# Kernel tuning notes

Hardware: AMD Instinct MI355X
Metric: run time of the kernel (lower is better)

Reference implementation:

```python
import jax, jax.numpy as jnp
import numpy as np

B, C, H, W = 8, 256, 64, 64
HEADS, PTS = 8, 4
HD = C // HEADS
CIN_G, CIN_S, COUT = 1024, 320, 320


def _sine_pe(c, h, w):
    # LoFTR-style 2D sinusoidal position encoding, returns [C,H,W]
    pe = np.zeros((c, h, w), dtype=np.float32)
    y = np.broadcast_to(np.arange(h, dtype=np.float32)[None, :, None], (1, h, w))
    x = np.broadcast_to(np.arange(w, dtype=np.float32)[None, None, :], (1, h, w))
    div = np.exp(np.arange(0, c // 2, 2, dtype=np.float32) * (-np.log(10000.0) / (c // 2)))[:, None, None]
    pe[0::4] = np.sin(x * div)
    pe[1::4] = np.cos(x * div)
    pe[2::4] = np.sin(y * div)
    pe[3::4] = np.cos(y * div)
    return jnp.asarray(pe)


def _ref_points(h, w):
    # faithful to source: meshgrid over (W,H) 'ij', stack (col,row), flatten w-major
    rows = np.linspace(0, 1, w, dtype=np.float32)
    cols = np.linspace(0, 1, h, dtype=np.float32)
    R, Cg = np.meshgrid(rows, cols, indexing='ij')  # [W,H]
    return jnp.asarray(np.stack([Cg, R], -1).reshape(-1, 2))  # [W*H,2]


PE = _sine_pe(C, H, W)
RP = _ref_points(H, W)


def conv1x1(x, w, b):
    return jnp.einsum('bchw,oc->bohw', x, w) + b[None, :, None, None]


def deform_attn(qf, vf, vp_w, vp_b, so_w, so_b, aw_w, aw_b, op_w, op_b):
    # qf: [B,Nq,C]  vf: [B,Nv,C]  (single level, H x W value map)
    Bn, Nq, Cc = qf.shape
    v = (vf @ vp_w + vp_b).reshape(Bn, -1, HEADS, HD).transpose(0, 2, 1, 3)  # [B,h,Nv,hd]
    off = (qf @ so_w + so_b).reshape(Bn, Nq, HEADS, PTS, 2)
    aw = jax.nn.softmax((qf @ aw_w + aw_b).reshape(Bn, Nq, HEADS, PTS), axis=-1)
    loc = RP[None, :, None, None, :] + off / jnp.array([W, H], qf.dtype)  # [B,Nq,h,P,2]
    # grid_sample align_corners=False, zero padding
    px = loc[..., 0] * W - 0.5
    py = loc[..., 1] * H - 0.5
    x0 = jnp.floor(px).astype(jnp.int32)
    y0 = jnp.floor(py).astype(jnp.int32)
    wx = px - x0
    wy = py - y0
    out = jnp.zeros((Bn, HEADS, Nq, PTS, HD), qf.dtype)
    for dx, dy, wgt in ((0, 0, (1 - wx) * (1 - wy)), (1, 0, wx * (1 - wy)),
                        (0, 1, (1 - wx) * wy), (1, 1, wx * wy)):
        xi = x0 + dx
        yi = y0 + dy
        valid = ((xi >= 0) & (xi < W) & (yi >= 0) & (yi < H)).astype(qf.dtype)
        idx = jnp.clip(yi, 0, H - 1) * W + jnp.clip(xi, 0, W - 1)  # [B,Nq,h,P]
        idx_h = idx.transpose(0, 2, 1, 3).reshape(Bn, HEADS, Nq * PTS)
        g = jnp.take_along_axis(v, idx_h[..., None], axis=2).reshape(Bn, HEADS, Nq, PTS, HD)
        out = out + g * (wgt * valid).transpose(0, 2, 1, 3)[..., None]
    o = (out * aw.transpose(0, 2, 1, 3)[..., None]).sum(3)  # [B,h,Nq,hd]
    o = o.transpose(0, 2, 1, 3).reshape(Bn, Nq, Cc)
    return o @ op_w + op_b + qf  # mmcv: output_proj + identity (dropout=eval)


def cross_attn(q, value, vp_w, vp_b, so_w, so_b, aw_w, aw_b, op_w, op_b):
    qp = q + PE[None]  # query += pe
    qf = qp.reshape(qp.shape[0], C, H * W).transpose(0, 2, 1)
    vf = value.reshape(value.shape[0], C, H * W).transpose(0, 2, 1)
    o = deform_attn(qf, vf, vp_w, vp_b, so_w, so_b, aw_w, aw_b, op_w, op_b)
    o = o.transpose(0, 2, 1).reshape(qp.shape)
    return o + qp


def setup_inputs() -> dict:
    key = jax.random.key(0)
    ks = jax.random.split(key, 40)
    inp = {}
    inp['ground'] = jax.random.normal(ks[0], (B, CIN_G, H, W), jnp.float32)
    inp['sat'] = jax.random.normal(ks[1], (B, CIN_S, H, W), jnp.float32)
    inp['osm'] = jax.random.normal(ks[2], (B, CIN_S, H, W), jnp.float32)
    i = [3]
    def p(name, shape, scale=0.02):
        inp[name] = jax.random.normal(ks[i[0]], shape, jnp.float32) * scale
        i[0] += 1
    p('gc_w', (C, CIN_G)); p('gc_b', (C,))
    p('sc_w', (C, CIN_S)); p('sc_b', (C,))
    p('up_w', (COUT, C)); p('up_b', (COUT,))
    p('a_w1', (C, 64)); p('a_b1', (64,))
    p('a_w2', (64, 1)); p('a_b2', (1,))
    for pre in ('sat_', 'osm_'):
        p(pre + 'vp_w', (C, C)); p(pre + 'vp_b', (C,))
        p(pre + 'so_w', (C, HEADS * PTS * 2)); p(pre + 'so_b', (HEADS * PTS * 2,))
        p(pre + 'aw_w', (C, HEADS * PTS)); p(pre + 'aw_b', (HEADS * PTS,))
        p(pre + 'op_w', (C, C)); p(pre + 'op_b', (C,))
    inp['index'] = 0
    return inp


def reference(ground, sat, osm, gc_w, gc_b, sc_w, sc_b, up_w, up_b,
              a_w1, a_b1, a_w2, a_b2,
              sat_vp_w, sat_vp_b, sat_so_w, sat_so_b, sat_aw_w, sat_aw_b, sat_op_w, sat_op_b,
              osm_vp_w, osm_vp_b, osm_so_w, osm_so_b, osm_aw_w, osm_aw_b, osm_op_w, osm_op_b,
              index):
    del index  # params for index=0 already selected
    g = conv1x1(ground, gc_w, gc_b)
    s = conv1x1(sat, sc_w, sc_b)
    o = conv1x1(osm, sc_w, sc_b)  # source bug: osm projected with sat_convs
    gf = g.reshape(B, C, H * W).transpose(0, 2, 1)
    alpha = jax.nn.sigmoid(jax.nn.relu(gf @ a_w1 + a_b1) @ a_w2 + a_b2)  # [B,Nq,1]
    a = alpha.mean(axis=1)[:, :, None, None]  # [B,1,1,1]
    sat_out = cross_attn(g, s, sat_vp_w, sat_vp_b, sat_so_w, sat_so_b, sat_aw_w, sat_aw_b, sat_op_w, sat_op_b)
    # torch in-place `query += pe` inside ca_sat mutates `ground`, so ca_osm sees g + PE
    osm_out = cross_attn(g + PE[None], o, osm_vp_w, osm_vp_b, osm_so_w, osm_so_b, osm_aw_w, osm_aw_b, osm_op_w, osm_op_b)
    fused = a * sat_out + (1.0 - a) * osm_out
    return conv1x1(fused, up_w, up_b), a
```

## Files before the change

kernel.cpp:

```cpp
#include <hip/hip_runtime.h>
#include <cstddef>
#include <cstdint>

#define NB 8
#define NQ 4096

typedef __attribute__((ext_vector_type(8))) short bfrag8;
typedef __attribute__((ext_vector_type(4))) float facc4;
typedef __attribute__((ext_vector_type(4))) unsigned short us4;
typedef __attribute__((ext_vector_type(8))) unsigned short us8;

__device__ __forceinline__ float bf2f(unsigned short u) {
  union { unsigned int i; float f; } v; v.i = ((unsigned int)u) << 16; return v.f;
}
__device__ __forceinline__ unsigned short f2bf(float f) {
  union { float f; unsigned int i; } v; v.f = f;
  unsigned int r = v.i + 0x7FFFu + ((v.i >> 16) & 1u);
  return (unsigned short)(r >> 16);
}
__device__ __forceinline__ void gload16(const void* g, void* l) {
  __builtin_amdgcn_global_load_lds(
      (const __attribute__((address_space(1))) void*)g,
      (__attribute__((address_space(3))) void*)l, 16, 0, 0);
}

struct PrepArgs {
  const float *gc_w, *up_w, *up_b;
  const float *so_w0, *so_b0, *so_w1, *so_b1;
  const float *aw_w0, *aw_b0, *aw_w1, *aw_b1;
  const float *op_w0, *op_w1;
  unsigned short *PET, *WG, *WUP, *OPT0, *OPT1, *SOW0, *SOW1;
  float *BUPP, *SOB0, *SOB1;
};

__global__ __launch_bounds__(256) void mega_prep(PrepArgs p) {
  const int blk = blockIdx.x, t = threadIdx.x;
  if (blk < 4096) {
    int idx = blk * 256 + t;
    int q = idx >> 8, c = idx & 255;
    int h = q >> 6, w = q & 63;
    int k = c >> 2, m = c & 3;
    float dv = expf((float)(2 * k) * (-9.210340371976184f / 128.0f));
    float arg = ((m < 2) ? (float)w : (float)h) * dv;
    p.PET[idx] = f2bf(((m & 1) == 0) ? sinf(arg) : cosf(arg));
  } else if (blk < 5120) {
    int i = (blk - 4096) * 256 + t;
    p.WG[i] = f2bf(p.gc_w[i]);
  } else if (blk < 5504) {
    int i = (blk - 5120) * 256 + t;
    int m = i >> 8, k = i & 255;
    p.WUP[i] = (m < 320) ? f2bf(p.up_w[m * 256 + k]) : 0;
  } else if (blk < 5505) {
    p.BUPP[t] = (t < 320) ? p.up_b[t] : 0.f;
    if (t < 128) {
      int i2 = 256 + t;
      p.BUPP[i2] = (i2 < 320) ? p.up_b[i2] : 0.f;
    }
  } else if (blk < 6017) {
    int i = (blk - 5505) * 256 + t;
    int which = i >> 16, j = i & 65535;
    int o = j >> 8, k = j & 255;
    (which ? p.OPT1 : p.OPT0)[j] = f2bf((which ? p.op_w1 : p.op_w0)[k * 256 + o]);
  } else {
    int i = (blk - 6017) * 256 + t;
    int which = i >> 15, j = i & 32767;
    int row = j >> 8, k = j & 255;
    const float* sw = which ? p.so_w1 : p.so_w0;
    const float* aw = which ? p.aw_w1 : p.aw_w0;
    float v = 0.f;
    if (row < 64) v = sw[k * 64 + row];
    else if (row < 96) v = aw[k * 32 + (row - 64)];
    (which ? p.SOW1 : p.SOW0)[j] = f2bf(v);
    if (j < 128) {
      const float* sb = which ? p.so_b1 : p.so_b0;
      const float* ab = which ? p.aw_b1 : p.aw_b0;
      (which ? p.SOB1 : p.SOB0)[j] = (j < 64) ? sb[j] : ((j < 96) ? ab[j - 64] : 0.f);
    }
  }
}

__global__ __launch_bounds__(256) void k_wv(const float* __restrict__ vp_w0,
                                            const float* __restrict__ vp_b0,
                                            const float* __restrict__ vp_w1,
                                            const float* __restrict__ vp_b1,
                                            const float* __restrict__ sc_w,
                                            const float* __restrict__ sc_b,
                                            unsigned short* __restrict__ WV0,
                                            unsigned short* __restrict__ WV1,
                                            float* __restrict__ BV0,
                                            float* __restrict__ BV1) {
  const int br = blockIdx.y, kt = blockIdx.x, k0 = kt * 20, t = threadIdx.x;
  const float* vp = br ? vp_w1 : vp_w0;
  unsigned short* WV = br ? WV1 : WV0;
  __shared__ float vt[32][256];
  __shared__ float st[32][20];
  __shared__ float sb[32];
  float acc[20] = {};
  float accB = 0.f;
  for (int c0 = 0; c0 < 256; c0 += 32) {
    __syncthreads();
#pragma unroll
    for (int cc = 0; cc < 32; ++cc)
      vt[cc][t] = vp[(size_t)(c0 + cc) * 256 + t];
    for (int i = t; i < 640; i += 256)
      st[i / 20][i % 20] = sc_w[(size_t)(c0 + i / 20) * 320 + k0 + (i % 20)];
    if (t < 32) sb[t] = sc_b[c0 + t];
    __syncthreads();
#pragma unroll
    for (int cc = 0; cc < 32; ++cc) {
      float v = vt[cc][t];
      accB = fmaf(v, sb[cc], accB);
#pragma unroll
      for (int j = 0; j < 20; ++j)
        acc[j] = fmaf(v, st[cc][j], acc[j]);
    }
  }
#pragma unroll
  for (int j = 0; j < 20; ++j) WV[(size_t)t * 320 + k0 + j] = f2bf(acc[j]);
  if (kt == 0) (br ? BV1 : BV0)[t] = (br ? vp_b1 : vp_b0)[t] + accB;
}

struct GArgs {
  const unsigned short* W[2];
  const unsigned short* X[2];
  const float* bias[2];
  void* out[2];
  const unsigned short* res[2];
  float rscale[2];
  int K, ldm, bmask, brshift;
};
template <int MODE>
__global__ __launch_bounds__(256) void gemm_bf16(GArgs g) {
  __shared__ unsigned short As[8192];
  __shared__ unsigned short Bs[8192];
  const int t = threadIdx.x;
  const int lane = t & 63, w = t >> 6;
  const int z = blockIdx.z;
  const int b = z & g.bmask, br = z >> g.brshift;
  const int K = g.K;
  const int n0 = blockIdx.x * 128, m0 = 0;
  const unsigned short* W = g.W[br];
  const unsigned short* Xb = g.X[br] + (size_t)b * NQ * K;

  const unsigned short* asrc[4];
  const unsigned short* bsrc[4];
  unsigned short* adst[4];
  unsigned short* bdst[4];
#pragma unroll
  for (int i = 0; i < 4; ++i) {
    int cid = i * 256 + t;
    int row = cid >> 3;
    int cc = (cid & 7) ^ (row & 7);
    asrc[i] = W + (size_t)(m0 + row) * K + cc * 8;
    bsrc[i] = Xb + (size_t)(n0 + row) * K + cc * 8;
    adst[i] = &As[i * 2048 + w * 512];
    bdst[i] = &Bs[i * 2048 + w * 512];
  }
  const int wm = (w >> 1) * 64, wn = (w & 1) * 64;
  const int l15 = lane & 15, l4 = lane >> 4;
  facc4 acc[4][4];
#pragma unroll
  for (int i = 0; i < 4; ++i)
#pragma unroll
    for (int j = 0; j < 4; ++j) acc[i][j] = facc4{0.f, 0.f, 0.f, 0.f};

  for (int k0 = 0; k0 < K; k0 += 64) {
    if (k0) __syncthreads();
#pragma unroll
    for (int i = 0; i < 4; ++i) {
      gload16(asrc[i], adst[i]);
      gload16(bsrc[i], bdst[i]);
      asrc[i] += 64; bsrc[i] += 64;
    }
    __syncthreads();
#pragma unroll
    for (int kk = 0; kk < 2; ++kk) {
      bfrag8 af[4], bf[4];
#pragma unroll
      for (int mi = 0; mi < 4; ++mi) {
        int row = wm + mi * 16 + l15;
        af[mi] = *reinterpret_cast<const bfrag8*>(&As[row * 64 + (((kk * 4 + l4) ^ (row & 7)) * 8)]);
      }
#pragma unroll
      for (int ni = 0; ni < 4; ++ni) {
        int row = wn + ni * 16 + l15;
        bf[ni] = *reinterpret_cast<const bfrag8*>(&Bs[row * 64 + (((kk * 4 + l4) ^ (row & 7)) * 8)]);
      }
#pragma unroll
      for (int mi = 0; mi < 4; ++mi)
#pragma unroll
        for (int ni = 0; ni < 4; ++ni)
          acc[mi][ni] = __builtin_amdgcn_mfma_f32_16x16x32_bf16(af[mi], bf[ni], acc[mi][ni], 0, 0, 0);
    }
  }
  const size_t bq = (size_t)b * NQ;
#pragma unroll
  for (int mi = 0; mi < 4; ++mi) {
#pragma unroll
    for (int ni = 0; ni < 4; ++ni) {
      int m = m0 + wm + mi * 16 + l4 * 4;
      int n = n0 + wn + ni * 16 + l15;
      facc4 v = acc[mi][ni];
      unsigned short* o16 = (unsigned short*)g.out[br];
      float rv[4] = {v[0], v[1], v[2], v[3]};
      if constexpr (MODE == 1) {
        float sc = g.rscale[br];
        float4 bv = *reinterpret_cast<const float4*>(&g.bias[br][m]);
        rv[0] = rv[0] * sc + bv.x; rv[1] = rv[1] * sc + bv.y;
        rv[2] = rv[2] * sc + bv.z; rv[3] = rv[3] * sc + bv.w;
      }
      if constexpr (MODE == 2) {
        float sc = g.rscale[br];
        us4 rr = *reinterpret_cast<const us4*>(&g.res[br][(size_t)n * 128 + m]);
#pragma unroll
        for (int r = 0; r < 4; ++r) rv[r] += sc * bf2f(rr[r]);
      }
      us4 pk;
#pragma unroll
      for (int r = 0; r < 4; ++r) pk[r] = f2bf(rv[r]);
      *reinterpret_cast<us4*>(&o16[(bq + n) * g.ldm + m]) = pk;
    }
  }
}

struct NArgs {
  const unsigned short* W[2];
  const void* X[2];
  const float* bias[2];
  void* out[2];
  const unsigned short* G;
  const unsigned short* PET;
  const float* afin;
  float rs[2];
  int K, zmask, zshift;
};
template <int BSRC, int MODE>
__global__ __launch_bounds__(256) void gemm_n64(NArgs g) {
  __shared__ unsigned short As[16384];
  __shared__ unsigned short Bs[4096];
  const int t = threadIdx.x;
  const int lane = t & 63, w = t >> 6;
  const int z = blockIdx.z;
  const int b = z & g.zmask, br = z >> g.zshift;
  const int K = g.K;
  const int n0 = blockIdx.x * 64;

  const unsigned short* W = g.W[br];
  const unsigned short* asrc[8];
  unsigned short* adst[8];
#pragma unroll
  for (int i = 0; i < 8; ++i) {
    int c = t + 256 * i;
    int row = c >> 3;
    int k8 = (c & 7) ^ (row & 7);
    asrc[i] = W + (size_t)row * K + k8 * 8;
    adst[i] = &As[w * 512 + i * 2048];
  }

  const unsigned short* bsrc16[2];
  unsigned short* bdst16[2];
  const float* bsrcf = nullptr;
  const int kb = t >> 4, nb = t & 15;
  if constexpr (BSRC == 0) {
    const unsigned short* Xh = (const unsigned short*)g.X[br];
#pragma unroll
    for (int i = 0; i < 2; ++i) {
      int c = t + 256 * i;
      int n = c >> 3;
      int k8 = (c & 7) ^ (n & 7);
      bsrc16[i] = Xh + ((size_t)b * NQ + n0 + n) * K + k8 * 8;
      bdst16[i] = &Bs[w * 512 + i * 2048];
    }
  } else {
    const float* Xf = (const float*)g.X[br];
    bsrcf = Xf + (size_t)b * K * NQ + (size_t)(kb * 4) * NQ + n0 + nb * 4;
  }

  const int l15 = lane & 15, l4 = lane >> 4;
  facc4 acc[4][4];
#pragma unroll
  for (int i = 0; i < 4; ++i)
#pragma unroll
    for (int j = 0; j < 4; ++j) acc[i][j] = facc4{0.f, 0.f, 0.f, 0.f};

  for (int k0 = 0; k0 < K; k0 += 64) {
    if (k0) __syncthreads();
#pragma unroll
    for (int i = 0; i < 8; ++i) {
      gload16(asrc[i], adst[i]);
      asrc[i] += 64;
    }
    if constexpr (BSRC == 0) {
      gload16(bsrc16[0], bdst16[0]); bsrc16[0] += 64;
      gload16(bsrc16[1], bdst16[1]); bsrc16[1] += 64;
    } else {
      float vv[4][4];
#pragma unroll
      for (int r = 0; r < 4; ++r) {
        float4 v = *reinterpret_cast<const float4*>(bsrcf + (size_t)k0 * NQ + (size_t)r * NQ);
        vv[r][0] = v.x; vv[r][1] = v.y; vv[r][2] = v.z; vv[r][3] = v.w;
      }
#pragma unroll
      for (int c = 0; c < 4; ++c) {
        int n = nb * 4 + c;
        us4 pk;
        pk[0] = f2bf(vv[0][c]); pk[1] = f2bf(vv[1][c]);
        pk[2] = f2bf(vv[2][c]); pk[3] = f2bf(vv[3][c]);
        int off = n * 64 + (((kb >> 1) ^ (n & 7)) * 8) + (kb & 1) * 4;
        *reinterpret_cast<us4*>(&Bs[off]) = pk;
      }
    }
    __syncthreads();
#pragma unroll
    for (int kk = 0; kk < 2; ++kk) {
      bfrag8 af[4], bf[4];
#pragma unroll
      for (int mi = 0; mi < 4; ++mi) {
        int row = w * 64 + mi * 16 + l15;
        af[mi] = *reinterpret_cast<const bfrag8*>(&As[row * 64 + (((kk * 4 + l4) ^ (row & 7)) * 8)]);
      }
#pragma unroll
      for (int ni = 0; ni < 4; ++ni) {
        int row = ni * 16 + l15;
        bf[ni] = *reinterpret_cast<const bfrag8*>(&Bs[row * 64 + (((kk * 4 + l4) ^ (row & 7)) * 8)]);
      }
#pragma unroll
      for (int mi = 0; mi < 4; ++mi)
#pragma unroll
        for (int ni = 0; ni < 4; ++ni)
          acc[mi][ni] = __builtin_amdgcn_mfma_f32_16x16x32_bf16(af[mi], bf[ni], acc[mi][ni], 0, 0, 0);
    }
  }

  const size_t bq = (size_t)b * NQ;
  unsigned short* o16 = (unsigned short*)g.out[br];
#pragma unroll
  for (int mi = 0; mi < 4; ++mi) {
#pragma unroll
    for (int ni = 0; ni < 4; ++ni) {
      int m = w * 64 + mi * 16 + l4 * 4;
      int n = n0 + ni * 16 + l15;
      facc4 v = acc[mi][ni];
      float4 bv = *reinterpret_cast<const float4*>(&g.bias[br][m]);
      float rv[4] = {v[0] + bv.x, v[1] + bv.y, v[2] + bv.z, v[3] + bv.w};
      if constexpr (MODE == 6) {
        float a = g.afin[b];
        float s = br ? (1.f - a) : a;
        float rsc = g.rs[br];
        us4 gv = *reinterpret_cast<const us4*>(&g.G[(bq + n) * 256 + m]);
        us4 pv = *reinterpret_cast<const us4*>(&g.PET[(size_t)n * 256 + m]);
#pragma unroll
        for (int r = 0; r < 4; ++r)
          rv[r] = s * (rv[r] + 2.f * bf2f(gv[r]) + rsc * bf2f(pv[r]));
      }
      us4 pk;
#pragma unroll
      for (int r = 0; r < 4; ++r) pk[r] = f2bf(rv[r]);
      *reinterpret_cast<us4*>(&o16[(bq + n) * 256 + m]) = pk;
    }
  }
}

__global__ __launch_bounds__(384) void gemm_up(const unsigned short* __restrict__ W,
                                               const unsigned short* __restrict__ S0,
                                               const unsigned short* __restrict__ S1,
                                               const float* __restrict__ bias,
                                               float* __restrict__ out) {
  __shared__ unsigned short As[24576];
  __shared__ unsigned short Bs[4096];
  const int t = threadIdx.x;
  const int lane = t & 63, w = t >> 6;
  const int b = blockIdx.z;
  const int n0 = blockIdx.x * 64;

  const unsigned short* asrc[8];
  unsigned short* adst[8];
#pragma unroll
  for (int i = 0; i < 8; ++i) {
    int c = t + 384 * i;
    int row = c >> 3;
    int k8 = (c & 7) ^ (row & 7);
    asrc[i] = W + (size_t)row * 256 + k8 * 8;
    adst[i] = &As[w * 512 + i * 3072];
  }
  const bool bst = t < 256;
  size_t bidx[2];
  int bn[2];
  if (bst) {
#pragma unroll
    for (int i = 0; i < 2; ++i) {
      int c = t + 256 * i;
      bn[i] = c >> 3;
      int bk8 = (c & 7) ^ (bn[i] & 7);
      bidx[i] = ((size_t)b * NQ + n0 + bn[i]) * 256 + bk8 * 8;
    }
  }

  const int l15 = lane & 15, l4 = lane >> 4;
  facc4 acc[4][4];
#pragma unroll
  for (int i = 0; i < 4; ++i)
#pragma unroll
    for (int j = 0; j < 4; ++j) acc[i][j] = facc4{0.f, 0.f, 0.f, 0.f};

  for (int k0 = 0; k0 < 256; k0 += 64) {
    if (k0) __syncthreads();
#pragma unroll
    for (int i = 0; i < 8; ++i) {
      gload16(asrc[i], adst[i]);
      asrc[i] += 64;
    }
    if (bst) {
#pragma unroll
      for (int i = 0; i < 2; ++i) {
        us8 x = *reinterpret_cast<const us8*>(&S0[bidx[i] + k0]);
        us8 y = *reinterpret_cast<const us8*>(&S1[bidx[i] + k0]);
        us8 o;
#pragma unroll
        for (int j = 0; j < 8; ++j) o[j] = f2bf(bf2f(x[j]) + bf2f(y[j]));
        *reinterpret_cast<us8*>(&Bs[(t + 256 * i) * 8]) = o;
      }
    }
    __syncthreads();
#pragma unroll
    for (int kk = 0; kk < 2; ++kk) {
      bfrag8 af[4], bf[4];
#pragma unroll
      for (int mi = 0; mi < 4; ++mi) {
        int row = w * 64 + mi * 16 + l15;
        af[mi] = *reinterpret_cast<const bfrag8*>(&As[row * 64 + (((kk * 4 + l4) ^ (row & 7)) * 8)]);
      }
#pragma unroll
      for (int ni = 0; ni < 4; ++ni) {
        int row = ni * 16 + l15;
        bf[ni] = *reinterpret_cast<const bfrag8*>(&Bs[row * 64 + (((kk * 4 + l4) ^ (row & 7)) * 8)]);
      }
#pragma unroll
      for (int mi = 0; mi < 4; ++mi)
#pragma unroll
        for (int ni = 0; ni < 4; ++ni)
          acc[mi][ni] = __builtin_amdgcn_mfma_f32_16x16x32_bf16(af[mi], bf[ni], acc[mi][ni], 0, 0, 0);
    }
  }
#pragma unroll
  for (int mi = 0; mi < 4; ++mi) {
    int m = w * 64 + mi * 16 + l4 * 4;
    if (m >= 320) continue;
#pragma unroll
    for (int ni = 0; ni < 4; ++ni) {
      int n = n0 + ni * 16 + l15;
      facc4 v = acc[mi][ni];
#pragma unroll
      for (int r = 0; r < 4; ++r)
        out[((size_t)b * 320 + m + r) * NQ + n] = v[r] + bias[m + r];
    }
  }
}

__global__ __launch_bounds__(256) void k_alpha(const unsigned short* __restrict__ G,
                                               const float* __restrict__ w1,
                                               const float* __restrict__ b1,
                                               const float* __restrict__ w2,
                                               const float* __restrict__ b2,
                                               float* __restrict__ partial) {
  int b = blockIdx.y;
  int qbase = blockIdx.x * 16;
  __shared__ float gs[16][256];
  __shared__ float wsum[4];
  int t = threadIdx.x;
  const unsigned short* gp = G + ((size_t)b * NQ + qbase) * 256;
#pragma unroll
  for (int i = t; i < 512; i += 256) {
    bfrag8 v = *reinterpret_cast<const bfrag8*>(&gp[i * 8]);
    int row = i >> 5, col = (i & 31) * 8;
#pragma unroll
    for (int j = 0; j < 8; ++j) gs[row][col + j] = bf2f((unsigned short)v[j]);
  }
  __syncthreads();
  int wv = t >> 6, lane = t & 63;
  float a0 = 0.f, a1 = 0.f, a2 = 0.f, a3 = 0.f;
  const float* g0 = gs[wv * 4 + 0];
  const float* g1 = gs[wv * 4 + 1];
  const float* g2 = gs[wv * 4 + 2];
  const float* g3 = gs[wv * 4 + 3];
#pragma unroll 4
  for (int k = 0; k < 256; ++k) {
    float wk = w1[k * 64 + lane];
    a0 = fmaf(g0[k], wk, a0); a1 = fmaf(g1[k], wk, a1);
    a2 = fmaf(g2[k], wk, a2); a3 = fmaf(g3[k], wk, a3);
  }
  float b1l = b1[lane], w2l = w2[lane];
  a0 = fmaxf(a0 + b1l, 0.f) * w2l; a1 = fmaxf(a1 + b1l, 0.f) * w2l;
  a2 = fmaxf(a2 + b1l, 0.f) * w2l; a3 = fmaxf(a3 + b1l, 0.f) * w2l;
#pragma unroll
  for (int off = 32; off; off >>= 1) {
    a0 += __shfl_xor(a0, off); a1 += __shfl_xor(a1, off);
    a2 += __shfl_xor(a2, off); a3 += __shfl_xor(a3, off);
  }
  if (lane == 0) {
    float bb = b2[0];
    float s = 1.f / (1.f + expf(-(a0 + bb))) + 1.f / (1.f + expf(-(a1 + bb))) +
              1.f / (1.f + expf(-(a2 + bb))) + 1.f / (1.f + expf(-(a3 + bb)));
    wsum[wv] = s;
  }
  __syncthreads();
  if (t == 0) partial[(size_t)b * 256 + blockIdx.x] = wsum[0] + wsum[1] + wsum[2] + wsum[3];
}

__global__ __launch_bounds__(256) void k_alpha_fin(const float* __restrict__ partial,
                                                   float* __restrict__ afin,
                                                   float* __restrict__ out_a) {
  int b = blockIdx.x;
  __shared__ float sm[256];
  sm[threadIdx.x] = partial[(size_t)b * 256 + threadIdx.x];
  __syncthreads();
  for (int st = 128; st; st >>= 1) {
    if (threadIdx.x < st) sm[threadIdx.x] += sm[threadIdx.x + st];
    __syncthreads();
  }
  if (threadIdx.x == 0) {
    float a = sm[0] * (1.f / 4096.f);
    afin[b] = a;
    out_a[b] = a;
  }
}

__global__ __launch_bounds__(256) void k_sample(const unsigned short* __restrict__ VP0,
                                                const unsigned short* __restrict__ VP1,
                                                const unsigned short* __restrict__ SWb,
                                                unsigned short* __restrict__ OATT0,
                                                unsigned short* __restrict__ OATT1) {
  int y = blockIdx.y;
  int b = y & 7, br = y >> 3;
  int q0 = blockIdx.x * 8;
  const unsigned short* VP = (br ? VP1 : VP0) + (size_t)b * NQ * 256;
  const unsigned short* SWp = SWb + (((size_t)br * NB + b) * NQ + q0) * 128;
  unsigned short* OATT = (br ? OATT1 : OATT0) + ((size_t)b * NQ + q0) * 256;
  __shared__ unsigned short sws[1024];
  int t = threadIdx.x;
  *reinterpret_cast<us4*>(&sws[t * 4]) = *reinterpret_cast<const us4*>(&SWp[t * 4]);
  __syncthreads();
  int qi = t >> 5, ss = t & 31, head = ss >> 2, hdg = ss & 3;
  int q = q0 + qi;
  const unsigned short* sw = &sws[qi * 128];
  float l0 = bf2f(sw[64 + head * 4 + 0]);
  float l1 = bf2f(sw[64 + head * 4 + 1]);
  float l2 = bf2f(sw[64 + head * 4 + 2]);
  float l3 = bf2f(sw[64 + head * 4 + 3]);
  float mx = fmaxf(fmaxf(l0, l1), fmaxf(l2, l3));
  float e0 = expf(l0 - mx), e1 = expf(l1 - mx), e2 = expf(l2 - mx), e3 = expf(l3 - mx);
  float inv = 1.f / (e0 + e1 + e2 + e3);
  float aw[4] = {e0 * inv, e1 * inv, e2 * inv, e3 * inv};
  float rpx = (float)(q & 63) * (64.f / 63.f) - 0.5f;
  float rpy = (float)(q >> 6) * (64.f / 63.f) - 0.5f;
  const unsigned short* vb = VP + head * 32 + hdg * 8;
  float acc[8] = {};
#pragma unroll
  for (int p = 0; p < 4; ++p) {
    float px = rpx + bf2f(sw[head * 8 + p * 2 + 0]);
    float py = rpy + bf2f(sw[head * 8 + p * 2 + 1]);
    float fx = floorf(px), fy = floorf(py);
    int x0 = (int)fx, y0 = (int)fy;
    float wx = px - fx, wy = py - fy;
#pragma unroll
    for (int dy = 0; dy < 2; ++dy) {
#pragma unroll
      for (int dx = 0; dx < 2; ++dx) {
        int xi = x0 + dx, yi = y0 + dy;
        if (xi >= 0 && xi < 64 && yi >= 0 && yi < 64) {
          float wa = aw[p] * (dx ? wx : 1.f - wx) * (dy ? wy : 1.f - wy);
          bfrag8 v = *reinterpret_cast<const bfrag8*>(&vb[(size_t)(yi * 64 + xi) * 256]);
#pragma unroll
          for (int j = 0; j < 8; ++j) acc[j] = fmaf(wa, bf2f((unsigned short)v[j]), acc[j]);
        }
      }
    }
  }
  us8 o;
#pragma unroll
  for (int j = 0; j < 8; ++j) o[j] = f2bf(acc[j]);
  *reinterpret_cast<us8*>(&OATT[qi * 256 + ss * 8]) = o;
}

extern "C" void kernel_launch(void* const* d_in, const int* in_sizes, int n_in,
                              void* d_out, int out_size, void* d_ws, size_t ws_size,
                              hipStream_t stream) {
  const float* ground = (const float*)d_in[0];
  const float* sat = (const float*)d_in[1];
  const float* osm = (const float*)d_in[2];
  const float* gc_w = (const float*)d_in[3];
  const float* gc_b = (const float*)d_in[4];
  const float* sc_w = (const float*)d_in[5];
  const float* sc_b = (const float*)d_in[6];
  const float* up_w = (const float*)d_in[7];
  const float* up_b = (const float*)d_in[8];
  const float* a_w1 = (const float*)d_in[9];
  const float* a_b1 = (const float*)d_in[10];
  const float* a_w2 = (const float*)d_in[11];
  const float* a_b2 = (const float*)d_in[12];
  const float* vp_w[2] = {(const float*)d_in[13], (const float*)d_in[21]};
  const float* vp_b[2] = {(const float*)d_in[14], (const float*)d_in[22]};
  const float* so_w[2] = {(const float*)d_in[15], (const float*)d_in[23]};
  const float* so_b[2] = {(const float*)d_in[16], (const float*)d_in[24]};
  const float* aw_w[2] = {(const float*)d_in[17], (const float*)d_in[25]};
  const float* aw_b[2] = {(const float*)d_in[18], (const float*)d_in[26]};
  const float* op_w[2] = {(const float*)d_in[19], (const float*)d_in[27]};
  const float* op_b[2] = {(const float*)d_in[20], (const float*)d_in[28]};

  char* wsb = (char*)d_ws;
  const size_t MBy = 1 << 20;
  unsigned short* PET  = (unsigned short*)(wsb);
  unsigned short* WG   = (unsigned short*)(wsb + 2 * MBy);
  unsigned short* WV0  = (unsigned short*)(wsb + 2 * MBy + 524288);
  unsigned short* WV1  = (unsigned short*)(wsb + 2 * MBy + 786432);
  unsigned short* WUP  = (unsigned short*)(wsb + 3 * MBy);
  unsigned short* OPT0 = (unsigned short*)(wsb + 3 * MBy + 262144);
  unsigned short* OPT1 = (unsigned short*)(wsb + 3 * MBy + 393216);
  unsigned short* SOW0 = (unsigned short*)(wsb + 3 * MBy + 524288);
  unsigned short* SOW1 = (unsigned short*)(wsb + 3 * MBy + 589824);
  unsigned short* PESO0 = (unsigned short*)(wsb + 4 * MBy);
  unsigned short* PESO1 = (unsigned short*)(wsb + 5 * MBy);
  float* SOB0 = (float*)(wsb + 6 * MBy);
  float* SOB1 = (float*)(wsb + 6 * MBy + 4096);
  float* BV0  = (float*)(wsb + 6 * MBy + 8192);
  float* BV1  = (float*)(wsb + 6 * MBy + 12288);
  float* BUPP = (float*)(wsb + 6 * MBy + 16384);
  float* PART = (float*)(wsb + 6 * MBy + 32768);
  float* AFIN = (float*)(wsb + 6 * MBy + 65536);
  unsigned short* G     = (unsigned short*)(wsb + 8 * MBy);
  unsigned short* VP0b  = (unsigned short*)(wsb + 24 * MBy);
  unsigned short* VP1b  = (unsigned short*)(wsb + 40 * MBy);
  unsigned short* SW    = (unsigned short*)(wsb + 56 * MBy);
  unsigned short* OATT0 = (unsigned short*)(wsb + 72 * MBy);
  unsigned short* OATT1 = (unsigned short*)(wsb + 88 * MBy);
  unsigned short* SATO  = (unsigned short*)(wsb + 104 * MBy);
  unsigned short* OSMO  = (unsigned short*)(wsb + 120 * MBy);

  float* out32 = (float*)d_out;
  float* out_a = out32 + (size_t)NB * 320 * NQ;

  dim3 blk(256);

  {
    PrepArgs p;
    p.gc_w = gc_w; p.up_w = up_w; p.up_b = up_b;
    p.so_w0 = so_w[0]; p.so_b0 = so_b[0]; p.so_w1 = so_w[1]; p.so_b1 = so_b[1];
    p.aw_w0 = aw_w[0]; p.aw_b0 = aw_b[0]; p.aw_w1 = aw_w[1]; p.aw_b1 = aw_b[1];
    p.op_w0 = op_w[0]; p.op_w1 = op_w[1];
    p.PET = PET; p.WG = WG; p.WUP = WUP;
    p.OPT0 = OPT0; p.OPT1 = OPT1; p.SOW0 = SOW0; p.SOW1 = SOW1;
    p.BUPP = BUPP; p.SOB0 = SOB0; p.SOB1 = SOB1;
    mega_prep<<<dim3(6273), blk, 0, stream>>>(p);
  }
  k_wv<<<dim3(16, 2), blk, 0, stream>>>(vp_w[0], vp_b[0], vp_w[1], vp_b[1],
                                        sc_w, sc_b, WV0, WV1, BV0, BV1);

  {
    GArgs a = {};
    a.W[0] = SOW0; a.W[1] = SOW1;
    a.X[0] = PET;  a.X[1] = PET;
    a.bias[0] = SOB0; a.bias[1] = SOB1;
    a.out[0] = PESO0; a.out[1] = PESO1;
    a.rscale[0] = 1.f; a.rscale[1] = 2.f;
    a.K = 256; a.ldm = 128; a.bmask = 0; a.brshift = 0;
    gemm_bf16<1><<<dim3(32, 1, 2), blk, 0, stream>>>(a);
  }

  {
    NArgs a = {};
    a.W[0] = WG; a.W[1] = WG;
    a.X[0] = ground; a.X[1] = ground;
    a.bias[0] = gc_b; a.bias[1] = gc_b;
    a.out[0] = G; a.out[1] = G;
    a.K = 1024; a.zmask = 7; a.zshift = 31;
    gemm_n64<1, 0><<<dim3(64, 1, NB), blk, 0, stream>>>(a);
  }

  k_alpha<<<dim3(256, NB), blk, 0, stream>>>(G, a_w1, a_b1, a_w2, a_b2, PART);
  k_alpha_fin<<<dim3(NB), blk, 0, stream>>>(PART, AFIN, out_a);

  {
    GArgs a = {};
    a.W[0] = SOW0; a.W[1] = SOW1;
    a.X[0] = G; a.X[1] = G;
    a.out[0] = SW; a.out[1] = SW + (size_t)NB * NQ * 128;
    a.res[0] = PESO0; a.res[1] = PESO1;
    a.rscale[0] = 1.f; a.rscale[1] = 1.f;
    a.K = 256; a.ldm = 128; a.bmask = 7; a.brshift = 3;
    gemm_bf16<2><<<dim3(32, 1, 16), blk, 0, stream>>>(a);
  }

  {
    NArgs a = {};
    a.W[0] = WV0; a.W[1] = WV1;
    a.X[0] = sat; a.X[1] = osm;
    a.bias[0] = BV0; a.bias[1] = BV1;
    a.out[0] = VP0b; a.out[1] = VP1b;
    a.K = 320; a.zmask = 7; a.zshift = 3;
    gemm_n64<1, 0><<<dim3(64, 1, 16), blk, 0, stream>>>(a);
  }

  k_sample<<<dim3(512, 16), blk, 0, stream>>>(VP0b, VP1b, SW, OATT0, OATT1);

  {
    NArgs a = {};
    a.W[0] = OPT0; a.W[1] = OPT1;
    a.X[0] = OATT0; a.X[1] = OATT1;
    a.bias[0] = op_b[0]; a.bias[1] = op_b[1];
    a.out[0] = SATO; a.out[1] = OSMO;
    a.G = G; a.PET = PET; a.afin = AFIN;
    a.rs[0] = 2.f; a.rs[1] = 4.f;
    a.K = 256; a.zmask = 7; a.zshift = 3;
    gemm_n64<0, 6><<<dim3(64, 1, 16), blk, 0, stream>>>(a);
  }

  gemm_up<<<dim3(64, 1, NB), dim3(384), 0, stream>>>(WUP, SATO, OSMO, BUPP, out32);
}
```

Measured before the change: 299.0 us.

## Fuse deformable sampling, output projection and branch blend into one tail kernel

Replaces the separate sampling kernel and the output-projection GEMM with a single kernel. It gathers bilinear samples into LDS, multiplies them by the projection weights for both branches, and writes the alpha-blended fused result. The final upsampling GEMM now loads one precomputed fused tensor directly into LDS instead of adding two branch outputs. This removes several large intermediate round-trips through global memory and two launches. In exchange the grid is much smaller and each block uses a lot of LDS, so latency hiding for the gather may suffer.

Result: slower. 385.5 us (+28.9%).

```diff
diff --git a/kernel.cpp b/kernel.cpp
--- a/kernel.cpp
+++ b/kernel.cpp
@@ -138,7 +138,7 @@
   const int z = blockIdx.z;
   const int b = z & g.bmask, br = z >> g.brshift;
   const int K = g.K;
-  const int n0 = blockIdx.x * 128, m0 = 0;
+  const int n0 = blockIdx.x * 128;
   const unsigned short* W = g.W[br];
   const unsigned short* Xb = g.X[br] + (size_t)b * NQ * K;
 
@@ -151,7 +151,7 @@
     int cid = i * 256 + t;
     int row = cid >> 3;
     int cc = (cid & 7) ^ (row & 7);
-    asrc[i] = W + (size_t)(m0 + row) * K + cc * 8;
+    asrc[i] = W + (size_t)row * K + cc * 8;
     bsrc[i] = Xb + (size_t)(n0 + row) * K + cc * 8;
     adst[i] = &As[i * 2048 + w * 512];
     bdst[i] = &Bs[i * 2048 + w * 512];
@@ -198,7 +198,7 @@
   for (int mi = 0; mi < 4; ++mi) {
 #pragma unroll
     for (int ni = 0; ni < 4; ++ni) {
-      int m = m0 + wm + mi * 16 + l4 * 4;
+      int m = wm + mi * 16 + l4 * 4;
       int n = n0 + wn + ni * 16 + l15;
       facc4 v = acc[mi][ni];
       unsigned short* o16 = (unsigned short*)g.out[br];
@@ -228,13 +228,8 @@
   const void* X[2];
   const float* bias[2];
   void* out[2];
-  const unsigned short* G;
-  const unsigned short* PET;
-  const float* afin;
-  float rs[2];
   int K, zmask, zshift;
 };
-template <int BSRC, int MODE>
 __global__ __launch_bounds__(256) void gemm_n64(NArgs g) {
   __shared__ unsigned short As[16384];
   __shared__ unsigned short Bs[4096];
@@ -257,24 +252,9 @@
     adst[i] = &As[w * 512 + i * 2048];
   }
 
-  const unsigned short* bsrc16[2];
-  unsigned short* bdst16[2];
-  const float* bsrcf = nullptr;
   const int kb = t >> 4, nb = t & 15;
-  if constexpr (BSRC == 0) {
-    const unsigned short* Xh = (const unsigned short*)g.X[br];
-#pragma unroll
-    for (int i = 0; i < 2; ++i) {
-      int c = t + 256 * i;
-      int n = c >> 3;
-      int k8 = (c & 7) ^ (n & 7);
-      bsrc16[i] = Xh + ((size_t)b * NQ + n0 + n) * K + k8 * 8;
-      bdst16[i] = &Bs[w * 512 + i * 2048];
-    }
-  } else {
-    const float* Xf = (const float*)g.X[br];
-    bsrcf = Xf + (size_t)b * K * NQ + (size_t)(kb * 4) * NQ + n0 + nb * 4;
-  }
+  const float* Xf = (const float*)g.X[br];
+  const float* bsrcf = Xf + (size_t)b * K * NQ + (size_t)(kb * 4) * NQ + n0 + nb * 4;
 
   const int l15 = lane & 15, l4 = lane >> 4;
   facc4 acc[4][4];
@@ -290,10 +270,7 @@
       gload16(asrc[i], adst[i]);
       asrc[i] += 64;
     }
-    if constexpr (BSRC == 0) {
-      gload16(bsrc16[0], bdst16[0]); bsrc16[0] += 64;
-      gload16(bsrc16[1], bdst16[1]); bsrc16[1] += 64;
-    } else {
+    {
       float vv[4][4];
 #pragma unroll
       for (int r = 0; r < 4; ++r) {
@@ -342,28 +319,161 @@
       int n = n0 + ni * 16 + l15;
       facc4 v = acc[mi][ni];
       float4 bv = *reinterpret_cast<const float4*>(&g.bias[br][m]);
-      float rv[4] = {v[0] + bv.x, v[1] + bv.y, v[2] + bv.z, v[3] + bv.w};
-      if constexpr (MODE == 6) {
-        float a = g.afin[b];
-        float s = br ? (1.f - a) : a;
-        float rsc = g.rs[br];
-        us4 gv = *reinterpret_cast<const us4*>(&g.G[(bq + n) * 256 + m]);
-        us4 pv = *reinterpret_cast<const us4*>(&g.PET[(size_t)n * 256 + m]);
-#pragma unroll
-        for (int r = 0; r < 4; ++r)
-          rv[r] = s * (rv[r] + 2.f * bf2f(gv[r]) + rsc * bf2f(pv[r]));
-      }
       us4 pk;
-#pragma unroll
-      for (int r = 0; r < 4; ++r) pk[r] = f2bf(rv[r]);
+      pk[0] = f2bf(v[0] + bv.x); pk[1] = f2bf(v[1] + bv.y);
+      pk[2] = f2bf(v[2] + bv.z); pk[3] = f2bf(v[3] + bv.w);
       *reinterpret_cast<us4*>(&o16[(bq + n) * 256 + m]) = pk;
     }
   }
 }
 
+struct TArgs {
+  const unsigned short *VP0, *VP1, *SWb, *OPT0, *OPT1;
+  const float *opb0, *opb1;
+  const unsigned short *G, *PET;
+  const float *afin;
+  unsigned short *FUSED;
+};
+
+__global__ __launch_bounds__(256) void k_tail(TArgs g) {
+  __shared__ unsigned short sws[8192];
+  __shared__ unsigned short P[16384];
+  __shared__ unsigned short As[16384];
+  const int t = threadIdx.x;
+  const int lane = t & 63, w = t >> 6;
+  const int b = blockIdx.y;
+  const int q0 = blockIdx.x * 64;
+  const int l15 = lane & 15, l4 = lane >> 4;
+
+  facc4 acc0[4][4], acc1[4][4];
+#pragma unroll
+  for (int i = 0; i < 4; ++i)
+#pragma unroll
+    for (int j = 0; j < 4; ++j) {
+      acc0[i][j] = facc4{0.f, 0.f, 0.f, 0.f};
+      acc1[i][j] = facc4{0.f, 0.f, 0.f, 0.f};
+    }
+
+  auto branch_pass = [&](int br, facc4 (&accR)[4][4]) {
+    __syncthreads();
+    const unsigned short* SWp = g.SWb + (((size_t)br * NB + b) * NQ + q0) * 128;
+#pragma unroll
+    for (int i = 0; i < 4; ++i) {
+      int idx = (t + 256 * i) * 8;
+      *reinterpret_cast<us8*>(&sws[idx]) = *reinterpret_cast<const us8*>(&SWp[idx]);
+    }
+    __syncthreads();
+    const unsigned short* VP = (br ? g.VP1 : g.VP0) + (size_t)b * NQ * 256;
+#pragma unroll
+    for (int i = 0; i < 8; ++i) {
+      int tau = t + 256 * i;
+      int qi = tau >> 5, seg = tau & 31, head = seg >> 2, hdg = seg & 3;
+      int q = q0 + qi;
+      const unsigned short* sw = &sws[qi * 128];
+      float l0 = bf2f(sw[64 + head * 4 + 0]);
+      float l1 = bf2f(sw[64 + head * 4 + 1]);
+      float l2 = bf2f(sw[64 + head * 4 + 2]);
+      float l3 = bf2f(sw[64 + head * 4 + 3]);
+      float mx = fmaxf(fmaxf(l0, l1), fmaxf(l2, l3));
+      float e0 = expf(l0 - mx), e1 = expf(l1 - mx), e2 = expf(l2 - mx), e3 = expf(l3 - mx);
+      float inv = 1.f / (e0 + e1 + e2 + e3);
+      float aw[4] = {e0 * inv, e1 * inv, e2 * inv, e3 * inv};
+      float rpx = (float)(q & 63) * (64.f / 63.f) - 0.5f;
+      float rpy = (float)(q >> 6) * (64.f / 63.f) - 0.5f;
+      const unsigned short* vb = VP + head * 32 + hdg * 8;
+      float accg[8] = {};
+#pragma unroll
+      for (int p = 0; p < 4; ++p) {
+        float px = rpx + bf2f(sw[head * 8 + p * 2 + 0]);
+        float py = rpy + bf2f(sw[head * 8 + p * 2 + 1]);
+        float fx = floorf(px), fy = floorf(py);
+        int x0 = (int)fx, y0 = (int)fy;
+        float wx = px - fx, wy = py - fy;
+#pragma unroll
+        for (int dy = 0; dy < 2; ++dy) {
+#pragma unroll
+          for (int dx = 0; dx < 2; ++dx) {
+            int xi = x0 + dx, yi = y0 + dy;
+            if (xi >= 0 && xi < 64 && yi >= 0 && yi < 64) {
+              float wa = aw[p] * (dx ? wx : 1.f - wx) * (dy ? wy : 1.f - wy);
+              bfrag8 v = *reinterpret_cast<const bfrag8*>(&vb[(size_t)(yi * 64 + xi) * 256]);
+#pragma unroll
+              for (int j = 0; j < 8; ++j) accg[j] = fmaf(wa, bf2f((unsigned short)v[j]), accg[j]);
+            }
+          }
+        }
+      }
+      us8 o;
+#pragma unroll
+      for (int j = 0; j < 8; ++j) o[j] = f2bf(accg[j]);
+      int kt = seg >> 3, k8 = seg & 7;
+      *reinterpret_cast<us8*>(&P[kt * 4096 + qi * 64 + ((k8 ^ (qi & 7)) * 8)]) = o;
+    }
+    const unsigned short* OPT = br ? g.OPT1 : g.OPT0;
+    for (int kt = 0; kt < 4; ++kt) {
+      __syncthreads();
+#pragma unroll
+      for (int i = 0; i < 8; ++i) {
+        int c = t + 256 * i;
+        int row = c >> 3;
+        int k8 = (c & 7) ^ (row & 7);
+        gload16(OPT + (size_t)row * 256 + kt * 64 + k8 * 8, &As[w * 512 + i * 2048]);
+      }
+      __syncthreads();
+#pragma unroll
+      for (int kk = 0; kk < 2; ++kk) {
+        bfrag8 af[4], bf[4];
+#pragma unroll
+        for (int mi = 0; mi < 4; ++mi) {
+          int row = w * 64 + mi * 16 + l15;
+          af[mi] = *reinterpret_cast<const bfrag8*>(&As[row * 64 + (((kk * 4 + l4) ^ (row & 7)) * 8)]);
+        }
+#pragma unroll
+        for (int ni = 0; ni < 4; ++ni) {
+          int row = ni * 16 + l15;
+          bf[ni] = *reinterpret_cast<const bfrag8*>(&P[kt * 4096 + row * 64 + (((kk * 4 + l4) ^ (row & 7)) * 8)]);
+        }
+#pragma unroll
+        for (int mi = 0; mi < 4; ++mi)
+#pragma unroll
+          for (int ni = 0; ni < 4; ++ni)
+            accR[mi][ni] = __builtin_amdgcn_mfma_f32_16x16x32_bf16(af[mi], bf[ni], accR[mi][ni], 0, 0, 0);
+      }
+    }
+  };
+  branch_pass(0, acc0);
+  branch_pass(1, acc1);
+
+  float a = g.afin[b];
+  const size_t bq = (size_t)b * NQ;
+#pragma unroll
+  for (int mi = 0; mi < 4; ++mi) {
+#pragma unroll
+    for (int ni = 0; ni < 4; ++ni) {
+      int m = w * 64 + mi * 16 + l4 * 4;
+      int n = q0 + ni * 16 + l15;
+      float4 b0 = *reinterpret_cast<const float4*>(&g.opb0[m]);
+      float4 b1 = *reinterpret_cast<const float4*>(&g.opb1[m]);
+      us4 gv = *reinterpret_cast<const us4*>(&g.G[(bq + n) * 256 + m]);
+      us4 pv = *reinterpret_cast<const us4*>(&g.PET[(size_t)n * 256 + m]);
+      facc4 v0 = acc0[mi][ni], v1 = acc1[mi][ni];
+      float bb0[4] = {b0.x, b0.y, b0.z, b0.w};
+      float bb1[4] = {b1.x, b1.y, b1.z, b1.w};
+      us4 pk;
+#pragma unroll
+      for (int r = 0; r < 4; ++r) {
+        float gg = 2.f * bf2f(gv[r]), pp = bf2f(pv[r]);
+        float r0 = v0[r] + bb0[r] + gg + 2.f * pp;
+        float r1 = v1[r] + bb1[r] + gg + 4.f * pp;
+        pk[r] = f2bf(a * r0 + (1.f - a) * r1);
+      }
+      *reinterpret_cast<us4*>(&g.FUSED[(bq + n) * 256 + m]) = pk;
+    }
+  }
+}
+
 __global__ __launch_bounds__(384) void gemm_up(const unsigned short* __restrict__ W,
-                                               const unsigned short* __restrict__ S0,
-                                               const unsigned short* __restrict__ S1,
+                                               const unsigned short* __restrict__ FUSED,
                                                const float* __restrict__ bias,
                                                float* __restrict__ out) {
   __shared__ unsigned short As[24576];
@@ -384,15 +494,16 @@
     adst[i] = &As[w * 512 + i * 3072];
   }
   const bool bst = t < 256;
-  size_t bidx[2];
-  int bn[2];
+  const unsigned short* bsrc[2];
+  unsigned short* bdst[2];
   if (bst) {
 #pragma unroll
     for (int i = 0; i < 2; ++i) {
       int c = t + 256 * i;
-      bn[i] = c >> 3;
-      int bk8 = (c & 7) ^ (bn[i] & 7);
-      bidx[i] = ((size_t)b * NQ + n0 + bn[i]) * 256 + bk8 * 8;
+      int n = c >> 3;
+      int k8 = (c & 7) ^ (n & 7);
+      bsrc[i] = FUSED + ((size_t)b * NQ + n0 + n) * 256 + k8 * 8;
+      bdst[i] = &Bs[w * 512 + i * 2048];
     }
   }
 
@@ -411,15 +522,8 @@
       asrc[i] += 64;
     }
     if (bst) {
-#pragma unroll
-      for (int i = 0; i < 2; ++i) {
-        us8 x = *reinterpret_cast<const us8*>(&S0[bidx[i] + k0]);
-        us8 y = *reinterpret_cast<const us8*>(&S1[bidx[i] + k0]);
-        us8 o;
-#pragma unroll
-        for (int j = 0; j < 8; ++j) o[j] = f2bf(bf2f(x[j]) + bf2f(y[j]));
-        *reinterpret_cast<us8*>(&Bs[(t + 256 * i) * 8]) = o;
-      }
+      gload16(bsrc[0], bdst[0]); bsrc[0] += 64;
+      gload16(bsrc[1], bdst[1]); bsrc[1] += 64;
     }
     __syncthreads();
 #pragma unroll
@@ -523,63 +627,6 @@
     afin[b] = a;
     out_a[b] = a;
   }
-}
-
-__global__ __launch_bounds__(256) void k_sample(const unsigned short* __restrict__ VP0,
-                                                const unsigned short* __restrict__ VP1,
-                                                const unsigned short* __restrict__ SWb,
-                                                unsigned short* __restrict__ OATT0,
-                                                unsigned short* __restrict__ OATT1) {
-  int y = blockIdx.y;
-  int b = y & 7, br = y >> 3;
-  int q0 = blockIdx.x * 8;
-  const unsigned short* VP = (br ? VP1 : VP0) + (size_t)b * NQ * 256;
-  const unsigned short* SWp = SWb + (((size_t)br * NB + b) * NQ + q0) * 128;
-  unsigned short* OATT = (br ? OATT1 : OATT0) + ((size_t)b * NQ + q0) * 256;
-  __shared__ unsigned short sws[1024];
-  int t = threadIdx.x;
-  *reinterpret_cast<us4*>(&sws[t * 4]) = *reinterpret_cast<const us4*>(&SWp[t * 4]);
-  __syncthreads();
-  int qi = t >> 5, ss = t & 31, head = ss >> 2, hdg = ss & 3;
-  int q = q0 + qi;
-  const unsigned short* sw = &sws[qi * 128];
-  float l0 = bf2f(sw[64 + head * 4 + 0]);
-  float l1 = bf2f(sw[64 + head * 4 + 1]);
-  float l2 = bf2f(sw[64 + head * 4 + 2]);
-  float l3 = bf2f(sw[64 + head * 4 + 3]);
-  float mx = fmaxf(fmaxf(l0, l1), fmaxf(l2, l3));
-  float e0 = expf(l0 - mx), e1 = expf(l1 - mx), e2 = expf(l2 - mx), e3 = expf(l3 - mx);
-  float inv = 1.f / (e0 + e1 + e2 + e3);
-  float aw[4] = {e0 * inv, e1 * inv, e2 * inv, e3 * inv};
-  float rpx = (float)(q & 63) * (64.f / 63.f) - 0.5f;
-  float rpy = (float)(q >> 6) * (64.f / 63.f) - 0.5f;
-  const unsigned short* vb = VP + head * 32 + hdg * 8;
-  float acc[8] = {};
-#pragma unroll
-  for (int p = 0; p < 4; ++p) {
-    float px = rpx + bf2f(sw[head * 8 + p * 2 + 0]);
-    float py = rpy + bf2f(sw[head * 8 + p * 2 + 1]);
-    float fx = floorf(px), fy = floorf(py);
-    int x0 = (int)fx, y0 = (int)fy;
-    float wx = px - fx, wy = py - fy;
-#pragma unroll
-    for (int dy = 0; dy < 2; ++dy) {
-#pragma unroll
-      for (int dx = 0; dx < 2; ++dx) {
-        int xi = x0 + dx, yi = y0 + dy;
-        if (xi >= 0 && xi < 64 && yi >= 0 && yi < 64) {
-          float wa = aw[p] * (dx ? wx : 1.f - wx) * (dy ? wy : 1.f - wy);
-          bfrag8 v = *reinterpret_cast<const bfrag8*>(&vb[(size_t)(yi * 64 + xi) * 256]);
-#pragma unroll
-          for (int j = 0; j < 8; ++j) acc[j] = fmaf(wa, bf2f((unsigned short)v[j]), acc[j]);
-        }
-      }
-    }
-  }
-  us8 o;
-#pragma unroll
-  for (int j = 0; j < 8; ++j) o[j] = f2bf(acc[j]);
-  *reinterpret_cast<us8*>(&OATT[qi * 256 + ss * 8]) = o;
 }
 
 extern "C" void kernel_launch(void* const* d_in, const int* in_sizes, int n_in,
@@ -631,10 +678,7 @@
   unsigned short* VP0b  = (unsigned short*)(wsb + 24 * MBy);
   unsigned short* VP1b  = (unsigned short*)(wsb + 40 * MBy);
   unsigned short* SW    = (unsigned short*)(wsb + 56 * MBy);
-  unsigned short* OATT0 = (unsigned short*)(wsb + 72 * MBy);
-  unsigned short* OATT1 = (unsigned short*)(wsb + 88 * MBy);
-  unsigned short* SATO  = (unsigned short*)(wsb + 104 * MBy);
-  unsigned short* OSMO  = (unsigned short*)(wsb + 120 * MBy);
+  unsigned short* FUSED = (unsigned short*)(wsb + 72 * MBy);
 
   float* out32 = (float*)d_out;
   float* out_a = out32 + (size_t)NB * 320 * NQ;
@@ -673,7 +717,7 @@
     a.bias[0] = gc_b; a.bias[1] = gc_b;
     a.out[0] = G; a.out[1] = G;
     a.K = 1024; a.zmask = 7; a.zshift = 31;
-    gemm_n64<1, 0><<<dim3(64, 1, NB), blk, 0, stream>>>(a);
+    gemm_n64<<<dim3(64, 1, NB), blk, 0, stream>>>(a);
   }
 
   k_alpha<<<dim3(256, NB), blk, 0, stream>>>(G, a_w1, a_b1, a_w2, a_b2, PART);
@@ -697,22 +741,18 @@
     a.bias[0] = BV0; a.bias[1] = BV1;
     a.out[0] = VP0b; a.out[1] = VP1b;
     a.K = 320; a.zmask = 7; a.zshift = 3;
-    gemm_n64<1, 0><<<dim3(64, 1, 16), blk, 0, stream>>>(a);
-  }
-
-  k_sample<<<dim3(512, 16), blk, 0, stream>>>(VP0b, VP1b, SW, OATT0, OATT1);
+    gemm_n64<<<dim3(64, 1, 16), blk, 0, stream>>>(a);
+  }
 
   {
-    NArgs a = {};
-    a.W[0] = OPT0; a.W[1] = OPT1;
-    a.X[0] = OATT0; a.X[1] = OATT1;
-    a.bias[0] = op_b[0]; a.bias[1] = op_b[1];
-    a.out[0] = SATO; a.out[1] = OSMO;
+    TArgs a;
+    a.VP0 = VP0b; a.VP1 = VP1b; a.SWb = SW;
+    a.OPT0 = OPT0; a.OPT1 = OPT1;
+    a.opb0 = op_b[0]; a.opb1 = op_b[1];
     a.G = G; a.PET = PET; a.afin = AFIN;
-    a.rs[0] = 2.f; a.rs[1] = 4.f;
-    a.K = 256; a.zmask = 7; a.zshift = 3;
-    gemm_n64<0, 6><<<dim3(64, 1, 16), blk, 0, stream>>>(a);
-  }
-
-  gemm_up<<<dim3(64, 1, NB), dim3(384), 0, stream>>>(WUP, SATO, OSMO, BUPP, out32);
-}
+    a.FUSED = FUSED;
+    k_tail<<<dim3(64, NB), blk, 0, stream>>>(a);
+  }
+
+  gemm_up<<<dim3(64, 1, NB), dim3(384), 0, stream>>>(WUP, FUSED, BUPP, out32);
+}
```
